# Kernel optimization log

Hardware: AMD Instinct MI355X
Metric: run time of the kernel (lower is better)

Reference implementation:

```python
import jax, jax.numpy as jnp
import numpy as np

B, R, C, NH = 8, 64, 256, 8
N = R * R            # 4096 tokens
HD = C // NH         # head dim 32
FF = 3               # focusing factor

def dwconv(x, w, b):
    # x: (B, C, H, W); w: (C, 1, kh, kw) depthwise
    y = jax.lax.conv_general_dilated(
        x, w, window_strides=(1, 1), padding='SAME',
        dimension_numbers=('NCHW', 'OIHW', 'NCHW'),
        feature_group_count=x.shape[1])
    return y + b[None, :, None, None]

def setup_inputs() -> dict:
    key = jax.random.key(0)
    ks = jax.random.split(key, 6)
    return {
        'qkv': jax.random.normal(ks[0], (3, B, N, C), jnp.float32),
        'pos_enc': jax.random.normal(ks[1], (1, N, C), jnp.float32) * 0.02,
        'scale': jax.random.normal(ks[2], (1, 1, C), jnp.float32) * 0.02,
        'w_v': jax.random.normal(ks[3], (C, 1, 3, 3), jnp.float32) * 0.1,
        'b_v': jnp.zeros((C,), jnp.float32),
        'w_dwc': jax.random.normal(ks[4], (HD, 1, 5, 5), jnp.float32) * 0.1,
        'b_dwc': jnp.zeros((HD,), jnp.float32),
    }

def reference(qkv, pos_enc, scale, w_v, b_v, w_dwc, b_dwc):
    q, k, v = qkv[0], qkv[1], qkv[2]          # each (B, N, C)
    # --- LePE: depthwise 3x3 conv on v over full channel dim ---
    v_img = v.transpose(0, 2, 1).reshape(B, C, R, R)
    lepe = dwconv(v_img, w_v, b_v)            # (B, C, R, R)
    lepe = lepe.reshape(B * NH, HD, N).transpose(0, 2, 1)   # (B*h, N, hd)
    v = v_img.reshape(B, C, N).transpose(0, 2, 1)           # (B, N, C)
    # --- focused kernelization ---
    k = k + pos_enc
    sc = jax.nn.softplus(scale)
    q = (jax.nn.relu(q) + 1e-6) / sc
    k = (jax.nn.relu(k) + 1e-6) / sc
    qn = jnp.linalg.norm(q, axis=-1, keepdims=True)
    kn = jnp.linalg.norm(k, axis=-1, keepdims=True)
    q = q ** FF
    k = k ** FF
    q = q / jnp.linalg.norm(q, axis=-1, keepdims=True) * qn
    k = k / jnp.linalg.norm(k, axis=-1, keepdims=True) * kn
    split = lambda x: x.reshape(B, N, NH, HD).transpose(0, 2, 1, 3).reshape(B * NH, N, HD)
    q, k, v = split(q), split(k), split(v)    # (B*h, N, hd)
    # --- linear attention (kv aggregation path: N >> hd) ---
    z = 1.0 / (jnp.einsum('bic,bc->bi', q, k.sum(axis=1)) + 1e-6)
    kv = jnp.einsum('bjc,bjd->bcd', k, v)     # (B*h, hd, hd)
    x = jnp.einsum('bic,bcd,bi->bid', q, kv, z)
    # --- dwc feature mixing on v per head ---
    fm = v.transpose(0, 2, 1).reshape(B * NH, HD, R, R)
    fm = dwconv(fm, w_dwc, b_dwc).reshape(B * NH, HD, N).transpose(0, 2, 1)
    x = x + fm + lepe
    x = x.reshape(B, NH, N, HD).transpose(0, 2, 1, 3).reshape(B, N, C)
    return x
```

## Files before the change

kernel.cpp:

```cpp
#include <hip/hip_runtime.h>
#include <math.h>

#define B_  8
#define R_  64
#define C_  256
#define NH_ 8
#define N_  4096
#define HD_ 32

__device__ __forceinline__ float softplus_rcp(float s) {
    return 1.f / __logf(1.f + __expf(s));
}

__device__ __forceinline__ void gload16_lds(const float* g, float* l) {
    __builtin_amdgcn_global_load_lds(
        (const __attribute__((address_space(1))) unsigned int*)g,
        (__attribute__((address_space(3))) unsigned int*)l, 16, 0, 0);
}

__global__ __launch_bounds__(256) void kernelKV8(
        const float* __restrict__ qkv, const float* __restrict__ pos,
        const float* __restrict__ scale,
        float* __restrict__ part, float* __restrict__ kspart) {
    __shared__ float smem[8448];
    float* rsc_s = smem + 8192;

    const int t    = threadIdx.x;
    const int wave = t >> 6, lane = t & 63;
    const int tk   = lane >> 5;
    const int lr   = lane & 31;
    const int blk  = blockIdx.x;
    const int tok0 = blk * 32;
    const int row  = wave * 2 + tk;

    rsc_s[t] = softplus_rcp(scale[t]);

    const size_t qbase = (size_t)tok0 * C_;
    const size_t koff  = (size_t)B_ * N_ * C_;
    const size_t voff  = (size_t)2 * B_ * N_ * C_;

    const int h  = t >> 5;
    const int l  = t & 31;
    const int cg = l & 7;
    const int dg = l >> 3;

    float acc[4][8];
    #pragma unroll
    for (int ii = 0; ii < 4; ii++)
        #pragma unroll
        for (int jj = 0; jj < 8; jj++) acc[ii][jj] = 0.f;
    float ksp[4] = {0.f, 0.f, 0.f, 0.f};

    float4 sk[2], sp[2];
    float  rs[8];

    auto LOAD = [&](int tt) {
        float* vdst = smem + 4096 + (tt & 1) * 2048;
        const int r0 = wave * 2;
        const size_t vsrc = voff + qbase + (size_t)(tt * 8 + r0) * C_;
        gload16_lds(qkv + vsrc + lane * 4,      vdst + r0 * 256 + lane * 4);
        gload16_lds(qkv + vsrc + C_ + lane * 4, vdst + (r0 + 1) * 256 + lane * 4);
        const int    nrow = tt * 8 + row;
        const size_t off  = qbase + (size_t)nrow * C_;
        const size_t poff = (size_t)((tok0 + nrow) & (N_ - 1)) * C_;
        sk[0] = *(const float4*)(qkv + koff + off + lr * 4);
        sk[1] = *(const float4*)(qkv + koff + off + 128 + lr * 4);
        sp[0] = *(const float4*)(pos + poff + lr * 4);
        sp[1] = *(const float4*)(pos + poff + 128 + lr * 4);
    };

    auto PROC = [&](int tt) {
        float* kf_s = smem + (tt & 1) * 2048;
        float kc[8];
        float sk2 = 0.f, sk6 = 0.f;
        #pragma unroll
        for (int j = 0; j < 2; j++) {
            const float ka[4] = {sk[j].x, sk[j].y, sk[j].z, sk[j].w};
            const float pa[4] = {sp[j].x, sp[j].y, sp[j].z, sp[j].w};
            #pragma unroll
            for (int e = 0; e < 4; e++) {
                const float r  = rs[j * 4 + e];
                const float kw = (fmaxf(ka[e] + pa[e], 0.f) + 1e-6f) * r;
                sk2 += kw * kw;
                const float k3 = kw * kw * kw;
                sk6 += k3 * k3;
                kc[j * 4 + e] = k3;
            }
        }
        #pragma unroll
        for (int m = 1; m < 32; m <<= 1) {
            sk2 += __shfl_xor(sk2, m, 64);
            sk6 += __shfl_xor(sk6, m, 64);
        }
        const float ks = sqrtf(sk2) * rsqrtf(sk6);
        #pragma unroll
        for (int j = 0; j < 2; j++) {
            const float4 kf4 = make_float4(kc[j*4+0] * ks, kc[j*4+1] * ks,
                                           kc[j*4+2] * ks, kc[j*4+3] * ks);
            *(float4*)&kf_s[row * 256 + j * 128 + lr * 4] = kf4;
        }
    };

    auto COMP = [&](int tt) {
        const float* kf_s = smem + (tt & 1) * 2048;
        const float* v_s  = smem + 4096 + (tt & 1) * 2048;
        const float* kfp = kf_s + h * HD_ + cg * 4;
        const float* vp  = v_s  + h * HD_ + dg * 8;
        #pragma unroll
        for (int nl = 0; nl < 8; nl++) {
            const float4 kr = *(const float4*)(kfp + nl * 256);
            const float4 va = *(const float4*)(vp  + nl * 256);
            const float4 vb = *(const float4*)(vp  + nl * 256 + 4);
            ksp[0] += kr.x;  ksp[1] += kr.y;
            ksp[2] += kr.z;  ksp[3] += kr.w;
            const float kk[4] = {kr.x, kr.y, kr.z, kr.w};
            const float vv[8] = {va.x, va.y, va.z, va.w,
                                 vb.x, vb.y, vb.z, vb.w};
            #pragma unroll
            for (int ii = 0; ii < 4; ii++)
                #pragma unroll
                for (int jj = 0; jj < 8; jj++)
                    acc[ii][jj] = fmaf(kk[ii], vv[jj], acc[ii][jj]);
        }
    };

    LOAD(0);
    __syncthreads();
    #pragma unroll
    for (int j = 0; j < 2; j++)
        *(float4*)&rs[j * 4] = *(const float4*)&rsc_s[j * 128 + lr * 4];
    PROC(0);
    LOAD(1);
    __syncthreads();
    #pragma unroll
    for (int tt = 0; tt < 4; tt++) {
        COMP(tt);
        if (tt < 3) PROC(tt + 1);
        __syncthreads();
        if (tt < 2) LOAD(tt + 2);
    }

    #pragma unroll
    for (int ii = 0; ii < 4; ii++) {
        const float4 a = make_float4(acc[ii][0], acc[ii][1], acc[ii][2], acc[ii][3]);
        const float4 b = make_float4(acc[ii][4], acc[ii][5], acc[ii][6], acc[ii][7]);
        const int base = h * 1024 + (cg * 4 + ii) * 32 + dg * 8;
        *(float4*)&smem[base]     = a;
        *(float4*)&smem[base + 4] = b;
    }
    if (dg == 0)
        *(float4*)&kspart[(size_t)blk * 256 + h * 32 + cg * 4] =
            make_float4(ksp[0], ksp[1], ksp[2], ksp[3]);
    __syncthreads();
    float* pdst = part + (size_t)blk * 8192;
    #pragma unroll
    for (int i = 0; i < 8; i++)
        *(float4*)&pdst[i * 1024 + t * 4] = *(const float4*)&smem[i * 1024 + t * 4];
}

__global__ __launch_bounds__(256) void kernelRQ(
        const float* __restrict__ qkv, const float* __restrict__ scale,
        const float* __restrict__ part, const float* __restrict__ kspart,
        float* __restrict__ kv_ws, float* __restrict__ ksum_ws,
        float* __restrict__ qs_arr) {
    const int t   = threadIdx.x;
    const int bid = blockIdx.x;

    if (bid < 256) {
        const int bh = bid >> 2, q = bid & 3;
        const int b  = bh >> 3, h = bh & 7;
        const float* p = part + (size_t)(b * 128) * 8192 + h * 1024 + q * 256 + t;
        float s = 0.f;
        #pragma unroll 4
        for (int j = 0; j < 128; j++) s += p[(size_t)j * 8192];
        kv_ws[bh * 1024 + q * 256 + t] = s;

        if (q == 0 && t < 32) {
            const float* kp = kspart + (size_t)(b * 128) * 256 + h * 32 + t;
            float s2 = 0.f;
            #pragma unroll 8
            for (int j = 0; j < 128; j++) s2 += kp[(size_t)j * 256];
            ksum_ws[bh * 32 + t] = s2;
        }
        return;
    }

    __shared__ float rsc_s[C_];
    rsc_s[t] = softplus_rcp(scale[t]);
    __syncthreads();

    const int wave = t >> 6, lane = t & 63;
    const int tk   = lane >> 4;
    const int lr   = lane & 15;
    const int tok0 = (bid - 256) * 64;

    float rs[16];
    #pragma unroll
    for (int j = 0; j < 4; j++)
        *(float4*)&rs[j * 4] = *(const float4*)&rsc_s[j * 64 + lr * 4];

    #pragma unroll
    for (int it = 0; it < 4; it++) {
        const int tok = tok0 + it * 16 + wave * 4 + tk;
        const float* src = qkv + (size_t)tok * C_;
        float sq2 = 0.f, sq6 = 0.f;
        #pragma unroll
        for (int j = 0; j < 4; j++) {
            const float4 q4 = *(const float4*)(src + j * 64 + lr * 4);
            const float qa[4] = {q4.x, q4.y, q4.z, q4.w};
            #pragma unroll
            for (int e = 0; e < 4; e++) {
                const float qv = (fmaxf(qa[e], 0.f) + 1e-6f) * rs[j * 4 + e];
                sq2 += qv * qv;
                const float q3 = qv * qv * qv;
                sq6 += q3 * q3;
            }
        }
        #pragma unroll
        for (int m = 1; m < 16; m <<= 1) {
            sq2 += __shfl_xor(sq2, m, 64);
            sq6 += __shfl_xor(sq6, m, 64);
        }
        if (lr == 0) qs_arr[tok] = sqrtf(sq2) * rsqrtf(sq6);
    }
}

__global__ __launch_bounds__(256) void kernelCD4(
        const float* __restrict__ qkv, const float* __restrict__ qs_arr,
        const float* __restrict__ kv_ws, const float* __restrict__ ksum_ws,
        const float* __restrict__ scale,
        const float* __restrict__ w_v,  const float* __restrict__ b_v,
        const float* __restrict__ w_dwc, const float* __restrict__ b_dwc,
        float* __restrict__ out) {
    __shared__ float v_s[20 * 20 * 32];
    __shared__ float rsc_s[32];
    const int t    = threadIdx.x;
    const int tile = blockIdx.x;
    const int h    = blockIdx.y;
    const int b    = blockIdx.z;
    const int ty0  = (tile >> 2) * 16, tx0 = (tile & 3) * 16;
    const int bh   = b * NH_ + h;

    const float4 kvr = ((const float4*)(kv_ws + (size_t)bh * 1024))[t];
    float ksr = 0.f;
    if (t < 32) {
        ksr      = ksum_ws[bh * HD_ + t];
        rsc_s[t] = softplus_rcp(scale[h * HD_ + t]);
    }

    const float* vb = qkv + (size_t)2 * B_ * N_ * C_ + (size_t)b * N_ * C_ + h * HD_;
    #pragma unroll
    for (int i = 0; i < 13; i++) {
        const int idx = i * 256 + t;
        if (idx < 3200) {
            const int pix = idx >> 3, d4 = (idx & 7) * 4;
            const int yy = pix / 20, xx = pix - yy * 20;
            const int gy = ty0 + yy - 2, gx = tx0 + xx - 2;
            float4 val = make_float4(0.f, 0.f, 0.f, 0.f);
            if (gy >= 0 && gy < R_ && gx >= 0 && gx < R_)
                val = *(const float4*)(vb + (size_t)(gy * R_ + gx) * C_ + d4);
            *(float4*)&v_s[pix * 32 + d4] = val;
        }
    }

    const int tyy = t >> 4, txx = t & 15;
    const int n_  = (ty0 + tyy) * R_ + (tx0 + txx);
    const int tok = b * N_ + n_;
    float qreg[32];
    {
        const float4* qsrc = (const float4*)(qkv + (size_t)tok * C_ + h * HD_);
        #pragma unroll
        for (int i = 0; i < 8; i++) ((float4*)qreg)[i] = qsrc[i];
    }
    const float qs = qs_arr[tok];

    const int c  = t & 31, pg = t >> 5;
    float wv[9], wd[25];
    {
        const float* wvp = w_v + (size_t)(h * HD_ + c) * 9;
        const float* wdp = w_dwc + (size_t)c * 25;
        #pragma unroll
        for (int i = 0; i < 9; i++)  wv[i] = wvp[i];
        #pragma unroll
        for (int i = 0; i < 25; i++) wd[i] = wdp[i];
    }
    const float bias = b_v[h * HD_ + c] + b_dwc[c];
    __syncthreads();

    float res[32];
    #pragma unroll
    for (int r2 = 0; r2 < 2; r2++) {
        const int ty = pg * 2 + r2;
        float win[5][5];
        #pragma unroll
        for (int j = 0; j < 5; j++)
            #pragma unroll
            for (int i = 0; i < 5; i++)
                win[j][i] = v_s[((ty + i) * 20 + j) * 32 + c];
        #pragma unroll
        for (int tx = 0; tx < 16; tx++) {
            float a = bias;
            #pragma unroll
            for (int j = 0; j < 5; j++) {
                const int slot = (tx + j) % 5;
                #pragma unroll
                for (int i = 0; i < 5; i++)
                    a = fmaf(wd[i * 5 + j], win[slot][i], a);
            }
            #pragma unroll
            for (int j = 1; j < 4; j++) {
                const int slot = (tx + j) % 5;
                #pragma unroll
                for (int i = 1; i < 4; i++)
                    a = fmaf(wv[(i - 1) * 3 + (j - 1)], win[slot][i], a);
            }
            res[r2 * 16 + tx] = a;
            if (tx < 15) {
                const int slot = tx % 5;
                #pragma unroll
                for (int i = 0; i < 5; i++)
                    win[slot][i] = v_s[((ty + i) * 20 + (tx + 5)) * 32 + c];
            }
        }
    }
    __syncthreads();
    #pragma unroll
    for (int r2 = 0; r2 < 2; r2++)
        #pragma unroll
        for (int tx = 0; tx < 16; tx++)
            v_s[((pg * 2 + r2) * 16 + tx) * 33 + c] = res[r2 * 16 + tx];
    *(float4*)&v_s[8448 + t * 4] = kvr;
    if (t < 32) v_s[9472 + t] = ksr;
    __syncthreads();

    {
        #pragma unroll
        for (int i = 0; i < 32; i++) {
            const float r = (fmaxf(qreg[i], 0.f) + 1e-6f) * rsc_s[i];
            qreg[i] = r * r * r * qs;
        }

        float denom = 1e-6f;
        #pragma unroll
        for (int cc = 0; cc < 32; cc++) denom = fmaf(qreg[cc], v_s[9472 + cc], denom);
        const float z = 1.f / denom;

        float o[32];
        #pragma unroll
        for (int i = 0; i < 32; i++) o[i] = 0.f;
        #pragma unroll
        for (int cc = 0; cc < 32; cc++) {
            const float qc = qreg[cc];
            #pragma unroll
            for (int d = 0; d < 32; d++)
                o[d] = fmaf(qc, v_s[8448 + cc * 32 + d], o[d]);
        }
        float4* dst = (float4*)(out + (size_t)tok * C_ + h * HD_);
        #pragma unroll
        for (int i = 0; i < 8; i++) {
            float4 v4;
            v4.x = fmaf(o[i*4+0], z, v_s[t * 33 + i*4+0]);
            v4.y = fmaf(o[i*4+1], z, v_s[t * 33 + i*4+1]);
            v4.z = fmaf(o[i*4+2], z, v_s[t * 33 + i*4+2]);
            v4.w = fmaf(o[i*4+3], z, v_s[t * 33 + i*4+3]);
            dst[i] = v4;
        }
    }
}

extern "C" void kernel_launch(void* const* d_in, const int* in_sizes, int n_in,
                              void* d_out, int out_size, void* d_ws, size_t ws_size,
                              hipStream_t stream) {
    const float* qkv   = (const float*)d_in[0];
    const float* pos   = (const float*)d_in[1];
    const float* scale = (const float*)d_in[2];
    const float* w_v   = (const float*)d_in[3];
    const float* b_v   = (const float*)d_in[4];
    const float* w_dwc = (const float*)d_in[5];
    const float* b_dwc = (const float*)d_in[6];
    float* out = (float*)d_out;

    float* qs_arr  = (float*)d_ws;
    float* part    = qs_arr + (size_t)B_ * N_;
    float* kspart  = part + (size_t)1024 * 8192;
    float* kv_ws   = kspart + (size_t)1024 * 256;
    float* ksum_ws = kv_ws + 64 * 1024;

    kernelKV8<<<dim3(1024), 256, 0, stream>>>(qkv, pos, scale, part, kspart);
    kernelRQ<<<dim3(768), 256, 0, stream>>>(qkv, scale, part, kspart,
                                            kv_ws, ksum_ws, qs_arr);
    kernelCD4<<<dim3(16, NH_, B_), 256, 0, stream>>>(qkv, qs_arr, kv_ws, ksum_ws,
                                                     scale, w_v, b_v, w_dwc, b_dwc, out);
}
```

Baseline: 232.4 us.

## Move convolutions into first kernel and add attention in a separate pass

The depthwise LePE and DWC convolutions now run as a role inside the first kernel, interleaved with the KV partial-sum and q-scale roles, so the convolution work overlaps the KV reduction instead of sitting after it. Convolution results are written to the output early. A new lightweight kernel then reads q, applies the kernel feature map, multiplies by the reduced KV matrix and accumulates into the output with a read-modify-write. The cost is an extra full-size read and write of the output, and the first kernel uses a larger shared-memory allocation, which may lower occupancy for the KV role.

```diff
diff --git a/kernel.cpp b/kernel.cpp
--- a/kernel.cpp
+++ b/kernel.cpp
@@ -18,19 +18,15 @@
         (__attribute__((address_space(3))) unsigned int*)l, 16, 0, 0);
 }
 
-__global__ __launch_bounds__(256) void kernelKV8(
+static __device__ __forceinline__ void roleKV(
         const float* __restrict__ qkv, const float* __restrict__ pos,
-        const float* __restrict__ scale,
-        float* __restrict__ part, float* __restrict__ kspart) {
-    __shared__ float smem[8448];
+        const float* __restrict__ scale, float* __restrict__ part,
+        float* __restrict__ kspart, float* smem, int kvb, int t) {
     float* rsc_s = smem + 8192;
-
-    const int t    = threadIdx.x;
     const int wave = t >> 6, lane = t & 63;
     const int tk   = lane >> 5;
     const int lr   = lane & 31;
-    const int blk  = blockIdx.x;
-    const int tok0 = blk * 32;
+    const int tok0 = kvb * 32;
     const int row  = wave * 2 + tk;
 
     rsc_s[t] = softplus_rcp(scale[t]);
@@ -149,104 +145,24 @@
         *(float4*)&smem[base + 4] = b;
     }
     if (dg == 0)
-        *(float4*)&kspart[(size_t)blk * 256 + h * 32 + cg * 4] =
+        *(float4*)&kspart[(size_t)kvb * 256 + h * 32 + cg * 4] =
             make_float4(ksp[0], ksp[1], ksp[2], ksp[3]);
     __syncthreads();
-    float* pdst = part + (size_t)blk * 8192;
+    float* pdst = part + (size_t)kvb * 8192;
     #pragma unroll
     for (int i = 0; i < 8; i++)
         *(float4*)&pdst[i * 1024 + t * 4] = *(const float4*)&smem[i * 1024 + t * 4];
 }
 
-__global__ __launch_bounds__(256) void kernelRQ(
-        const float* __restrict__ qkv, const float* __restrict__ scale,
-        const float* __restrict__ part, const float* __restrict__ kspart,
-        float* __restrict__ kv_ws, float* __restrict__ ksum_ws,
-        float* __restrict__ qs_arr) {
-    const int t   = threadIdx.x;
-    const int bid = blockIdx.x;
-
-    if (bid < 256) {
-        const int bh = bid >> 2, q = bid & 3;
-        const int b  = bh >> 3, h = bh & 7;
-        const float* p = part + (size_t)(b * 128) * 8192 + h * 1024 + q * 256 + t;
-        float s = 0.f;
-        #pragma unroll 4
-        for (int j = 0; j < 128; j++) s += p[(size_t)j * 8192];
-        kv_ws[bh * 1024 + q * 256 + t] = s;
-
-        if (q == 0 && t < 32) {
-            const float* kp = kspart + (size_t)(b * 128) * 256 + h * 32 + t;
-            float s2 = 0.f;
-            #pragma unroll 8
-            for (int j = 0; j < 128; j++) s2 += kp[(size_t)j * 256];
-            ksum_ws[bh * 32 + t] = s2;
-        }
-        return;
-    }
-
-    __shared__ float rsc_s[C_];
-    rsc_s[t] = softplus_rcp(scale[t]);
-    __syncthreads();
-
-    const int wave = t >> 6, lane = t & 63;
-    const int tk   = lane >> 4;
-    const int lr   = lane & 15;
-    const int tok0 = (bid - 256) * 64;
-
-    float rs[16];
-    #pragma unroll
-    for (int j = 0; j < 4; j++)
-        *(float4*)&rs[j * 4] = *(const float4*)&rsc_s[j * 64 + lr * 4];
-
-    #pragma unroll
-    for (int it = 0; it < 4; it++) {
-        const int tok = tok0 + it * 16 + wave * 4 + tk;
-        const float* src = qkv + (size_t)tok * C_;
-        float sq2 = 0.f, sq6 = 0.f;
-        #pragma unroll
-        for (int j = 0; j < 4; j++) {
-            const float4 q4 = *(const float4*)(src + j * 64 + lr * 4);
-            const float qa[4] = {q4.x, q4.y, q4.z, q4.w};
-            #pragma unroll
-            for (int e = 0; e < 4; e++) {
-                const float qv = (fmaxf(qa[e], 0.f) + 1e-6f) * rs[j * 4 + e];
-                sq2 += qv * qv;
-                const float q3 = qv * qv * qv;
-                sq6 += q3 * q3;
-            }
-        }
-        #pragma unroll
-        for (int m = 1; m < 16; m <<= 1) {
-            sq2 += __shfl_xor(sq2, m, 64);
-            sq6 += __shfl_xor(sq6, m, 64);
-        }
-        if (lr == 0) qs_arr[tok] = sqrtf(sq2) * rsqrtf(sq6);
-    }
-}
-
-__global__ __launch_bounds__(256) void kernelCD4(
-        const float* __restrict__ qkv, const float* __restrict__ qs_arr,
-        const float* __restrict__ kv_ws, const float* __restrict__ ksum_ws,
-        const float* __restrict__ scale,
+static __device__ __forceinline__ void roleCONV(
+        const float* __restrict__ qkv,
         const float* __restrict__ w_v,  const float* __restrict__ b_v,
         const float* __restrict__ w_dwc, const float* __restrict__ b_dwc,
-        float* __restrict__ out) {
-    __shared__ float v_s[20 * 20 * 32];
-    __shared__ float rsc_s[32];
-    const int t    = threadIdx.x;
-    const int tile = blockIdx.x;
-    const int h    = blockIdx.y;
-    const int b    = blockIdx.z;
+        float* __restrict__ out, float* v_s, int cb, int t) {
+    const int tile = cb & 15;
+    const int h    = (cb >> 4) & 7;
+    const int b    = cb >> 7;
     const int ty0  = (tile >> 2) * 16, tx0 = (tile & 3) * 16;
-    const int bh   = b * NH_ + h;
-
-    const float4 kvr = ((const float4*)(kv_ws + (size_t)bh * 1024))[t];
-    float ksr = 0.f;
-    if (t < 32) {
-        ksr      = ksum_ws[bh * HD_ + t];
-        rsc_s[t] = softplus_rcp(scale[h * HD_ + t]);
-    }
 
     const float* vb = qkv + (size_t)2 * B_ * N_ * C_ + (size_t)b * N_ * C_ + h * HD_;
     #pragma unroll
@@ -262,17 +178,6 @@
             *(float4*)&v_s[pix * 32 + d4] = val;
         }
     }
-
-    const int tyy = t >> 4, txx = t & 15;
-    const int n_  = (ty0 + tyy) * R_ + (tx0 + txx);
-    const int tok = b * N_ + n_;
-    float qreg[32];
-    {
-        const float4* qsrc = (const float4*)(qkv + (size_t)tok * C_ + h * HD_);
-        #pragma unroll
-        for (int i = 0; i < 8; i++) ((float4*)qreg)[i] = qsrc[i];
-    }
-    const float qs = qs_arr[tok];
 
     const int c  = t & 31, pg = t >> 5;
     float wv[9], wd[25];
@@ -329,42 +234,163 @@
         #pragma unroll
         for (int tx = 0; tx < 16; tx++)
             v_s[((pg * 2 + r2) * 16 + tx) * 33 + c] = res[r2 * 16 + tx];
-    *(float4*)&v_s[8448 + t * 4] = kvr;
-    if (t < 32) v_s[9472 + t] = ksr;
-    __syncthreads();
-
+    __syncthreads();
+
+    const int tyy = t >> 4, txx = t & 15;
+    const int tok = b * N_ + (ty0 + tyy) * R_ + (tx0 + txx);
+    float4* dst = (float4*)(out + (size_t)tok * C_ + h * HD_);
+    #pragma unroll
+    for (int i = 0; i < 8; i++) {
+        float4 v4;
+        v4.x = v_s[t * 33 + i*4+0];
+        v4.y = v_s[t * 33 + i*4+1];
+        v4.z = v_s[t * 33 + i*4+2];
+        v4.w = v_s[t * 33 + i*4+3];
+        dst[i] = v4;
+    }
+}
+
+static __device__ __forceinline__ void roleQS(
+        const float* __restrict__ qkv, const float* __restrict__ scale,
+        float* __restrict__ qs_arr, float* rsc_s, int qsb, int t) {
+    rsc_s[t] = softplus_rcp(scale[t]);
+    __syncthreads();
+
+    const int wave = t >> 6, lane = t & 63;
+    const int tk   = lane >> 4;
+    const int lr   = lane & 15;
+    const int tok0 = qsb * 64;
+
+    float rs[16];
+    #pragma unroll
+    for (int j = 0; j < 4; j++)
+        *(float4*)&rs[j * 4] = *(const float4*)&rsc_s[j * 64 + lr * 4];
+
+    #pragma unroll
+    for (int it = 0; it < 4; it++) {
+        const int tok = tok0 + it * 16 + wave * 4 + tk;
+        const float* src = qkv + (size_t)tok * C_;
+        float sq2 = 0.f, sq6 = 0.f;
+        #pragma unroll
+        for (int j = 0; j < 4; j++) {
+            const float4 q4 = *(const float4*)(src + j * 64 + lr * 4);
+            const float qa[4] = {q4.x, q4.y, q4.z, q4.w};
+            #pragma unroll
+            for (int e = 0; e < 4; e++) {
+                const float qv = (fmaxf(qa[e], 0.f) + 1e-6f) * rs[j * 4 + e];
+                sq2 += qv * qv;
+                const float q3 = qv * qv * qv;
+                sq6 += q3 * q3;
+            }
+        }
+        #pragma unroll
+        for (int m = 1; m < 16; m <<= 1) {
+            sq2 += __shfl_xor(sq2, m, 64);
+            sq6 += __shfl_xor(sq6, m, 64);
+        }
+        if (lr == 0) qs_arr[tok] = sqrtf(sq2) * rsqrtf(sq6);
+    }
+}
+
+__global__ __launch_bounds__(256) void kernelA(
+        const float* __restrict__ qkv, const float* __restrict__ pos,
+        const float* __restrict__ scale,
+        const float* __restrict__ w_v,  const float* __restrict__ b_v,
+        const float* __restrict__ w_dwc, const float* __restrict__ b_dwc,
+        float* __restrict__ out, float* __restrict__ qs_arr,
+        float* __restrict__ part, float* __restrict__ kspart) {
+    __shared__ float smem[12800];
+    const int t   = threadIdx.x;
+    const int blk = blockIdx.x;
+    if (blk >= 2048) {
+        roleQS(qkv, scale, qs_arr, smem, blk - 2048, t);
+    } else if (blk & 1) {
+        roleCONV(qkv, w_v, b_v, w_dwc, b_dwc, out, smem, blk >> 1, t);
+    } else {
+        roleKV(qkv, pos, scale, part, kspart, smem, blk >> 1, t);
+    }
+}
+
+__global__ __launch_bounds__(256) void kernelB(
+        const float* __restrict__ part, const float* __restrict__ kspart,
+        float* __restrict__ kv_ws, float* __restrict__ ksum_ws) {
+    const int t  = threadIdx.x;
+    const int bh = blockIdx.x >> 2, q = blockIdx.x & 3;
+    const int b  = bh >> 3, h = bh & 7;
+
+    const float* p = part + (size_t)(b * 128) * 8192 + h * 1024 + q * 256 + t;
+    float s = 0.f;
+    #pragma unroll 4
+    for (int j = 0; j < 128; j++) s += p[(size_t)j * 8192];
+    kv_ws[bh * 1024 + q * 256 + t] = s;
+
+    if (q == 0 && t < 32) {
+        const float* kp = kspart + (size_t)(b * 128) * 256 + h * 32 + t;
+        float s2 = 0.f;
+        #pragma unroll 8
+        for (int j = 0; j < 128; j++) s2 += kp[(size_t)j * 256];
+        ksum_ws[bh * 32 + t] = s2;
+    }
+}
+
+__global__ __launch_bounds__(256) void kernelC(
+        const float* __restrict__ qkv, const float* __restrict__ qs_arr,
+        const float* __restrict__ kv_ws, const float* __restrict__ ksum_ws,
+        const float* __restrict__ scale, float* __restrict__ out) {
+    __shared__ float kv_s[1024];
+    __shared__ float ks_s[32];
+    __shared__ float rsc_s[32];
+    const int t    = threadIdx.x;
+    const int tile = blockIdx.x & 15;
+    const int h    = (blockIdx.x >> 4) & 7;
+    const int b    = blockIdx.x >> 7;
+    const int bh   = b * NH_ + h;
+
+    ((float4*)kv_s)[t] = ((const float4*)(kv_ws + (size_t)bh * 1024))[t];
+    if (t < 32) {
+        ks_s[t]  = ksum_ws[bh * HD_ + t];
+        rsc_s[t] = softplus_rcp(scale[h * HD_ + t]);
+    }
+    __syncthreads();
+
+    const int tok = b * N_ + tile * 256 + t;
+    float q[32];
     {
-        #pragma unroll
-        for (int i = 0; i < 32; i++) {
-            const float r = (fmaxf(qreg[i], 0.f) + 1e-6f) * rsc_s[i];
-            qreg[i] = r * r * r * qs;
-        }
-
-        float denom = 1e-6f;
-        #pragma unroll
-        for (int cc = 0; cc < 32; cc++) denom = fmaf(qreg[cc], v_s[9472 + cc], denom);
-        const float z = 1.f / denom;
-
-        float o[32];
-        #pragma unroll
-        for (int i = 0; i < 32; i++) o[i] = 0.f;
-        #pragma unroll
-        for (int cc = 0; cc < 32; cc++) {
-            const float qc = qreg[cc];
-            #pragma unroll
-            for (int d = 0; d < 32; d++)
-                o[d] = fmaf(qc, v_s[8448 + cc * 32 + d], o[d]);
-        }
-        float4* dst = (float4*)(out + (size_t)tok * C_ + h * HD_);
-        #pragma unroll
-        for (int i = 0; i < 8; i++) {
-            float4 v4;
-            v4.x = fmaf(o[i*4+0], z, v_s[t * 33 + i*4+0]);
-            v4.y = fmaf(o[i*4+1], z, v_s[t * 33 + i*4+1]);
-            v4.z = fmaf(o[i*4+2], z, v_s[t * 33 + i*4+2]);
-            v4.w = fmaf(o[i*4+3], z, v_s[t * 33 + i*4+3]);
-            dst[i] = v4;
-        }
+        const float4* qsrc = (const float4*)(qkv + (size_t)tok * C_ + h * HD_);
+        #pragma unroll
+        for (int i = 0; i < 8; i++) ((float4*)q)[i] = qsrc[i];
+    }
+    const float qs = qs_arr[tok];
+    #pragma unroll
+    for (int i = 0; i < 32; i++) {
+        const float r = (fmaxf(q[i], 0.f) + 1e-6f) * rsc_s[i];
+        q[i] = r * r * r * qs;
+    }
+
+    float denom = 1e-6f;
+    #pragma unroll
+    for (int cc = 0; cc < 32; cc++) denom = fmaf(q[cc], ks_s[cc], denom);
+    const float z = 1.f / denom;
+
+    float o[32];
+    #pragma unroll
+    for (int i = 0; i < 32; i++) o[i] = 0.f;
+    #pragma unroll
+    for (int cc = 0; cc < 32; cc++) {
+        const float qc = q[cc];
+        #pragma unroll
+        for (int d = 0; d < 32; d++)
+            o[d] = fmaf(qc, kv_s[cc * 32 + d], o[d]);
+    }
+    float4* dst = (float4*)(out + (size_t)tok * C_ + h * HD_);
+    #pragma unroll
+    for (int i = 0; i < 8; i++) {
+        float4 cur = dst[i];
+        cur.x = fmaf(o[i*4+0], z, cur.x);
+        cur.y = fmaf(o[i*4+1], z, cur.y);
+        cur.z = fmaf(o[i*4+2], z, cur.z);
+        cur.w = fmaf(o[i*4+3], z, cur.w);
+        dst[i] = cur;
     }
 }
 
@@ -386,9 +412,10 @@
     float* kv_ws   = kspart + (size_t)1024 * 256;
     float* ksum_ws = kv_ws + 64 * 1024;
 
-    kernelKV8<<<dim3(1024), 256, 0, stream>>>(qkv, pos, scale, part, kspart);
-    kernelRQ<<<dim3(768), 256, 0, stream>>>(qkv, scale, part, kspart,
-                                            kv_ws, ksum_ws, qs_arr);
-    kernelCD4<<<dim3(16, NH_, B_), 256, 0, stream>>>(qkv, qs_arr, kv_ws, ksum_ws,
-                                                     scale, w_v, b_v, w_dwc, b_dwc, out);
-}
+    kernelA<<<dim3(2560), 256, 0, stream>>>(qkv, pos, scale, w_v, b_v,
+                                            w_dwc, b_dwc, out, qs_arr,
+                                            part, kspart);
+    kernelB<<<dim3(256), 256, 0, stream>>>(part, kspart, kv_ws, ksum_ws);
+    kernelC<<<dim3(1024), 256, 0, stream>>>(qkv, qs_arr, kv_ws, ksum_ws,
+                                            scale, out);
+}
```

Measured after the change: 264.8 us. 1.14x slower.
